# Kernel optimization log

Hardware: AMD Instinct MI355X
Metric: run time of the kernel (lower is better)

Reference implementation:

```python
import jax, jax.numpy as jnp
import numpy as np

B, N, M, D, H = 2, 2048, 77, 1024, 16
DH = D // H
SCALE = DH ** -0.5
EPS = 1e-5


def _round_ste(x):
    return x + jax.lax.stop_gradient(jnp.round(x) - x)


def _fq(x, delta, zp, n_bits):
    # UniformAffineQuantizer: fake quant-dequant with straight-through round
    xi = _round_ste(x / delta) + zp
    xq = jnp.clip(xi, 0.0, 2.0 ** n_bits - 1.0)
    return (xq - zp) * delta


def _ln(x, g, b):
    mu = jnp.mean(x, -1, keepdims=True)
    var = jnp.var(x, -1, keepdims=True)
    return (x - mu) * jax.lax.rsqrt(var + EPS) * g + b


def _attn(x, ctx, wq, wk, wv, wo, bo, dq, dk, dv, dw):
    b, n, _ = x.shape
    m = ctx.shape[1]
    q = (x @ wq).reshape(b, n, H, DH).transpose(0, 2, 1, 3)   # b h n d
    k = (ctx @ wk).reshape(b, m, H, DH).transpose(0, 2, 1, 3)
    v = (ctx @ wv).reshape(b, m, H, DH).transpose(0, 2, 1, 3)
    sim = jnp.einsum('bhid,bhjd->bhij', _fq(q, dq, 128.0, 8), _fq(k, dk, 128.0, 8)) * SCALE
    attn = jax.nn.softmax(sim, axis=-1)
    out = jnp.einsum('bhij,bhjd->bhid', _fq(attn, dw, 0.0, 8), _fq(v, dv, 128.0, 8))
    out = out.transpose(0, 2, 1, 3).reshape(b, n, D)
    return out @ wo + bo


def setup_inputs():
    key = jax.random.key(0)
    ks = jax.random.split(key, 16)
    w = lambda k, s: (jax.random.normal(k, s, jnp.float32) * 0.02)
    d = lambda v: jnp.full((1,), v, jnp.float32)
    return {
        'x': jax.random.normal(ks[0], (B, N, D), jnp.float32),
        'context': jax.random.normal(ks[1], (B, M, D), jnp.float32),
        'ln1_g': jnp.ones((D,), jnp.float32), 'ln1_b': jnp.zeros((D,), jnp.float32),
        'ln2_g': jnp.ones((D,), jnp.float32), 'ln2_b': jnp.zeros((D,), jnp.float32),
        'ln3_g': jnp.ones((D,), jnp.float32), 'ln3_b': jnp.zeros((D,), jnp.float32),
        'a1_wq': w(ks[2], (D, D)), 'a1_wk': w(ks[3], (D, D)), 'a1_wv': w(ks[4], (D, D)),
        'a1_wo': w(ks[5], (D, D)), 'a1_bo': jnp.zeros((D,), jnp.float32),
        'a2_wq': w(ks[6], (D, D)), 'a2_wk': w(ks[7], (D, D)), 'a2_wv': w(ks[8], (D, D)),
        'a2_wo': w(ks[9], (D, D)), 'a2_bo': jnp.zeros((D,), jnp.float32),
        'ff_w1': w(ks[10], (D, 8 * D)), 'ff_b1': jnp.zeros((8 * D,), jnp.float32),
        'ff_w2': w(ks[11], (4 * D, D)), 'ff_b2': jnp.zeros((D,), jnp.float32),
        'd_q1': d(0.02), 'd_k1': d(0.02), 'd_v1': d(0.02), 'd_w1': d(1.0 / 255.0),
        'd_q2': d(0.02), 'd_k2': d(0.02), 'd_v2': d(0.02), 'd_w2': d(1.0 / 255.0),
    }


def reference(x, context, ln1_g, ln1_b, ln2_g, ln2_b, ln3_g, ln3_b,
              a1_wq, a1_wk, a1_wv, a1_wo, a1_bo,
              a2_wq, a2_wk, a2_wv, a2_wo, a2_bo,
              ff_w1, ff_b1, ff_w2, ff_b2,
              d_q1, d_k1, d_v1, d_w1, d_q2, d_k2, d_v2, d_w2):
    # x = attn1(norm1(x)) + x   (self-attention)
    h1 = _ln(x, ln1_g, ln1_b)
    x = _attn(h1, h1, a1_wq, a1_wk, a1_wv, a1_wo, a1_bo, d_q1, d_k1, d_v1, d_w1) + x
    # x = attn2(norm2(x), context) + x   (cross-attention)
    h2 = _ln(x, ln2_g, ln2_b)
    x = _attn(h2, context, a2_wq, a2_wk, a2_wv, a2_wo, a2_bo, d_q2, d_k2, d_v2, d_w2) + x
    # x = ff(norm3(x)) + x   (GEGLU feed-forward)
    h3 = _ln(x, ln3_g, ln3_b)
    hg = h3 @ ff_w1 + ff_b1
    a, g = jnp.split(hg, 2, axis=-1)
    x = (a * jax.nn.gelu(g, approximate=False)) @ ff_w2 + ff_b2 + x
    return x
```

## Files before the change

kernel.cpp:

```cpp
#include <hip/hip_runtime.h>
#include <cstdint>
#include <cmath>

typedef unsigned short u16;
typedef unsigned int   u32;

typedef __bf16 bx8 __attribute__((ext_vector_type(8)));
typedef float  fx4 __attribute__((ext_vector_type(4)));

#define H_  16
#define DH_ 64
#define QSCALE 0.18033688011112042f

__device__ __forceinline__ float bf2f(u16 h){ return __uint_as_float(((u32)h) << 16); }
__device__ __forceinline__ u16 f2bf(float f){
  u32 u = __float_as_uint(f);
  u32 r = (u + 0x7FFFu + ((u >> 16) & 1u)) >> 16;
  return (u16)r;
}

__device__ __forceinline__ float ldv(const void* p, size_t i, int f32){
  return f32 ? ((const float*)p)[i] : bf2f(((const u16*)p)[i]);
}

__device__ __forceinline__ void gld16(const void* g, void* l){
  __builtin_amdgcn_global_load_lds((const __attribute__((address_space(1))) u32*)g,
                                   (__attribute__((address_space(3))) u32*)l,
                                   16, 0, 0);
}

__device__ __forceinline__ float fq_val(float v, float delta){
  float xi = rintf(v / delta) + 128.0f;
  xi = fminf(fmaxf(xi, 0.0f), 255.0f);
  return (xi - 128.0f) * delta;
}

__device__ __forceinline__ float gelu_f(float x){
  float x3 = x * x * x;
  float z = 0.7978845608028654f * x + 0.035677408136300125f * x3;
  float u = __expf(-2.0f * z);
  float t = 1.0f - 2.0f * u / (1.0f + u);
  return 0.5f * x * (1.0f + t);
}

__global__ void detect_k(const u32* __restrict__ x, int* __restrict__ flag){
  __shared__ int cnt;
  if (threadIdx.x == 0) cnt = 0;
  __syncthreads();
  u32 w = x[threadIdx.x];
  int e = (w >> 7) & 0xFF;
  if (e >= 100 && e <= 140) atomicAdd(&cnt, 1);
  __syncthreads();
  if (threadIdx.x == 0) *flag = (cnt < 192) ? 1 : 0;
}

__global__ __launch_bounds__(256) void cvt_k(const void* __restrict__ in, u16* __restrict__ out,
                                             int n, const int* __restrict__ flagp){
  int f32 = *flagp;
  int i = blockIdx.x * 256 + threadIdx.x;
  if (i < n) out[i] = f32 ? f2bf(((const float*)in)[i]) : ((const u16*)in)[i];
}

__global__ __launch_bounds__(256) void tr8_k(
    const void* s0, const void* s1, const void* s2, const void* s3,
    const void* s4, const void* s5, const void* s6, const void* s7,
    u16* __restrict__ out, const int* __restrict__ flagp){
  __shared__ u16 t[32][33];
  int f32 = *flagp;
  int z = blockIdx.z;
  const void* in = z==0?s0:z==1?s1:z==2?s2:z==3?s3:z==4?s4:z==5?s5:z==6?s6:s7;
  u16* o = out + ((size_t)z << 20);
  int n0 = blockIdx.x << 5, r0 = blockIdx.y << 5;
  int tx = threadIdx.x & 31, ty = threadIdx.x >> 5;
  #pragma unroll
  for (int i = 0; i < 4; i++)
    t[ty + i*8][tx] = f2bf(ldv(in, (size_t)(r0 + ty + i*8) * 1024 + n0 + tx, f32));
  __syncthreads();
  #pragma unroll
  for (int i = 0; i < 4; i++)
    o[(size_t)(n0 + ty + i*8) * 1024 + r0 + tx] = t[tx][ty + i*8];
}

__global__ __launch_bounds__(256) void tr_k(const void* __restrict__ in, u16* __restrict__ out,
                                            int Rout, int C, const int* __restrict__ flagp){
  __shared__ u16 t[32][33];
  int f32 = *flagp;
  int n0 = blockIdx.x << 5, r0 = blockIdx.y << 5;
  int tx = threadIdx.x & 31, ty = threadIdx.x >> 5;
  #pragma unroll
  for (int i = 0; i < 4; i++)
    t[ty + i*8][tx] = f2bf(ldv(in, (size_t)(r0 + ty + i*8) * C + n0 + tx, f32));
  __syncthreads();
  #pragma unroll
  for (int i = 0; i < 4; i++)
    out[(size_t)(n0 + ty + i*8) * Rout + r0 + tx] = t[tx][ty + i*8];
}

__global__ __launch_bounds__(256) void ln_k(const void* __restrict__ x,
    const void* __restrict__ gam, const void* __restrict__ bet, u16* __restrict__ out,
    const int* __restrict__ flagp, int xdual){
  __shared__ float sb[8];
  const int f32 = *flagp;
  const int f32x = xdual ? f32 : 0;
  const int row = blockIdx.x, t = threadIdx.x;
  float v0, v1, v2, v3;
  if (f32x){
    float4 xv = *(const float4*)((const float*)x + (size_t)row * 1024 + t * 4);
    v0 = xv.x; v1 = xv.y; v2 = xv.z; v3 = xv.w;
  } else {
    ushort4 xv = *(const ushort4*)((const u16*)x + (size_t)row * 1024 + t * 4);
    v0 = bf2f(xv.x); v1 = bf2f(xv.y); v2 = bf2f(xv.z); v3 = bf2f(xv.w);
  }
  float s = v0 + v1 + v2 + v3;
  #pragma unroll
  for (int mk = 32; mk; mk >>= 1) s += __shfl_xor(s, mk);
  if ((t & 63) == 0) sb[t >> 6] = s;
  __syncthreads();
  float mu = (sb[0] + sb[1] + sb[2] + sb[3]) * 0.0009765625f;
  float d0 = v0 - mu, d1 = v1 - mu, d2 = v2 - mu, d3 = v3 - mu;
  float ss = d0*d0 + d1*d1 + d2*d2 + d3*d3;
  #pragma unroll
  for (int mk = 32; mk; mk >>= 1) ss += __shfl_xor(ss, mk);
  if ((t & 63) == 0) sb[4 + (t >> 6)] = ss;
  __syncthreads();
  float var = (sb[4] + sb[5] + sb[6] + sb[7]) * 0.0009765625f;
  float rs = rsqrtf(var + 1e-5f);
  int c = t * 4;
  u16 o0 = f2bf(d0 * rs * ldv(gam, c+0, f32) + ldv(bet, c+0, f32));
  u16 o1 = f2bf(d1 * rs * ldv(gam, c+1, f32) + ldv(bet, c+1, f32));
  u16 o2 = f2bf(d2 * rs * ldv(gam, c+2, f32) + ldv(bet, c+2, f32));
  u16 o3 = f2bf(d3 * rs * ldv(gam, c+3, f32) + ldv(bet, c+3, f32));
  uint2 ov; ov.x = (u32)o0 | ((u32)o1 << 16); ov.y = (u32)o2 | ((u32)o3 << 16);
  *(uint2*)(out + (size_t)row * 1024 + c) = ov;
}

__global__ __launch_bounds__(512)
void gemm_mr(const u16* __restrict__ A, const u16* __restrict__ BT,
             u16* __restrict__ P0, u16* __restrict__ P1, u16* __restrict__ P2,
             const void* D0, const void* D1, const void* D2,
             float sc0, float sc1, float sc2,
             int md0, int md1, int md2,
             const int* __restrict__ flagp,
             int M, int K, int rpb, int npad)
{
  __shared__ u16 As[2][128 * 32];
  __shared__ u16 Bs[2][128 * 32];
  const int tid = threadIdx.x;
  const int l = tid & 63, w = tid >> 6;
  const int lr = l & 15, lq = l >> 4;
  const int m0 = blockIdx.y * 128, n0 = blockIdx.x * 128;
  const int wrow = (w & 3) * 32, wcol = (w >> 2) * 64;

  fx4 acc[2][4];
  #pragma unroll
  for (int i = 0; i < 2; i++)
    #pragma unroll
    for (int j = 0; j < 4; j++){ fx4 z = {0.f,0.f,0.f,0.f}; acc[i][j] = z; }

  const int r0 = tid >> 2, p0 = tid & 3;
  const int c0 = p0 ^ (r0 & 3);
  int am0 = m0 + r0; if (am0 > M - 1) am0 = M - 1;
  const u16* gA = A  + (size_t)am0 * K + c0 * 8;
  const u16* gB = BT + (size_t)(n0 + r0) * K + c0 * 8;
  const int lo = w * 512;

  const int nk = K >> 5;
  gld16(gA, &As[0][lo]);
  gld16(gB, &Bs[0][lo]);

  for (int kt = 0; kt < nk; ++kt){
    __syncthreads();
    const int cur = kt & 1;
    if (kt + 1 < nk){
      const int nb = cur ^ 1;
      const int ko = (kt + 1) << 5;
      gld16(gA + ko, &As[nb][lo]);
      gld16(gB + ko, &Bs[nb][lo]);
    }
    bx8 aF[2], bF[4];
    #pragma unroll
    for (int i = 0; i < 2; i++){
      int row = wrow + i * 16 + lr;
      aF[i] = *(const bx8*)&As[cur][row * 32 + (lq ^ (row & 3)) * 8];
    }
    #pragma unroll
    for (int j = 0; j < 4; j++){
      int row = wcol + j * 16 + lr;
      bF[j] = *(const bx8*)&Bs[cur][row * 32 + (lq ^ (row & 3)) * 8];
    }
    #pragma unroll
    for (int i = 0; i < 2; i++)
      #pragma unroll
      for (int j = 0; j < 4; j++)
        acc[i][j] = __builtin_amdgcn_mfma_f32_16x16x32_bf16(aF[i], bF[j], acc[i][j], 0, 0, 0);
  }

  const int f32 = *flagp;
  const int reg = n0 >> 10;
  const int cbase = n0 & 1023;
  u16* P = reg == 0 ? P0 : (reg == 1 ? P1 : P2);
  const void* D = reg == 0 ? D0 : (reg == 1 ? D1 : D2);
  const float sc = reg == 0 ? sc0 : (reg == 1 ? sc1 : sc2);
  const int md = reg == 0 ? md0 : (reg == 1 ? md1 : md2);
  const float delta = ldv(D, 0, f32);

  #pragma unroll
  for (int i = 0; i < 2; i++)
    #pragma unroll
    for (int j = 0; j < 4; j++)
      #pragma unroll
      for (int rr = 0; rr < 4; rr++){
        int gm = m0 + wrow + i * 16 + lq * 4 + rr;
        int col = cbase + wcol + j * 16 + lr;
        if (gm < M){
          float v = fq_val(acc[i][j][rr], delta) * sc;
          if (md == 0){
            P[(size_t)gm * 1024 + col] = f2bf(v);
          } else {
            int bb = gm / rpb; int jj = gm - bb * rpb;
            int hh = col >> 6, dh = col & 63;
            P[(size_t)((bb * H_ + hh) * DH_ + dh) * npad + jj] = f2bf(v);
          }
        }
      }
}

template<int MODE>
__global__ __launch_bounds__(256)
void gemm64(const u16* __restrict__ A, const u16* __restrict__ BT,
            void* __restrict__ Co, const void* __restrict__ res,
            const void* __restrict__ bias, const void* __restrict__ dptr, float sc,
            const int* __restrict__ flagp, int res_dual,
            int M, int K)
{
  __shared__ u16 As[2][64 * 32];
  __shared__ u16 Bs[2][128 * 32];
  const int tid = threadIdx.x;
  const int l = tid & 63, w = tid >> 6;
  const int lr = l & 15, lq = l >> 4;
  const int m0 = blockIdx.y * 64, n0 = blockIdx.x * 128;
  const int wrow = (w >> 1) * 32, wcol = (w & 1) * 64;

  fx4 acc[2][4];
  #pragma unroll
  for (int i = 0; i < 2; i++)
    #pragma unroll
    for (int j = 0; j < 4; j++){ fx4 z = {0.f,0.f,0.f,0.f}; acc[i][j] = z; }

  const int r0 = tid >> 2, p0 = tid & 3;
  const int c0 = p0 ^ (r0 & 3);
  const int r1 = r0 + 64;
  int am0 = m0 + r0; if (am0 > M - 1) am0 = M - 1;
  const u16* gA0 = A  + (size_t)am0 * K + c0 * 8;
  const u16* gB0 = BT + (size_t)(n0 + r0) * K + c0 * 8;
  const u16* gB1 = BT + (size_t)(n0 + r1) * K + c0 * 8;
  const int lo0 = (w * 64) * 8, lo1 = (256 + w * 64) * 8;

  const int nk = K >> 5;
  gld16(gA0, &As[0][lo0]);
  gld16(gB0, &Bs[0][lo0]);
  gld16(gB1, &Bs[0][lo1]);

  for (int kt = 0; kt < nk; ++kt){
    __syncthreads();
    const int cur = kt & 1;
    if (kt + 1 < nk){
      const int nb = cur ^ 1;
      const int ko = (kt + 1) << 5;
      gld16(gA0 + ko, &As[nb][lo0]);
      gld16(gB0 + ko, &Bs[nb][lo0]);
      gld16(gB1 + ko, &Bs[nb][lo1]);
    }
    bx8 aF[2], bF[4];
    #pragma unroll
    for (int i = 0; i < 2; i++){
      int row = wrow + i * 16 + lr;
      aF[i] = *(const bx8*)&As[cur][row * 32 + (lq ^ (row & 3)) * 8];
    }
    #pragma unroll
    for (int j = 0; j < 4; j++){
      int row = wcol + j * 16 + lr;
      bF[j] = *(const bx8*)&Bs[cur][row * 32 + (lq ^ (row & 3)) * 8];
    }
    #pragma unroll
    for (int i = 0; i < 2; i++)
      #pragma unroll
      for (int j = 0; j < 4; j++)
        acc[i][j] = __builtin_amdgcn_mfma_f32_16x16x32_bf16(aF[i], bF[j], acc[i][j], 0, 0, 0);
  }

  const int f32 = *flagp;
  float delta = 1.f;
  if (MODE == 0) delta = ldv(dptr, 0, f32);

  #pragma unroll
  for (int i = 0; i < 2; i++)
    #pragma unroll
    for (int j = 0; j < 4; j++)
      #pragma unroll
      for (int rr = 0; rr < 4; rr++){
        int gm = m0 + wrow + i * 16 + lq * 4 + rr;
        int gn = n0 + wcol + j * 16 + lr;
        if (gm < M){
          float v = acc[i][j][rr];
          size_t idx = (size_t)gm * 1024 + gn;
          if (MODE == 0){
            ((u16*)Co)[idx] = f2bf(fq_val(v, delta) * sc);
          } else if (MODE == 5){
            float r = res_dual ? ldv(res, idx, f32) : bf2f(((const u16*)res)[idx]);
            ((u16*)Co)[idx] = f2bf(v + ldv(bias, gn, f32) + r);
          } else {
            float o = v + ldv(bias, gn, f32) + bf2f(((const u16*)res)[idx]);
            if (f32) ((float*)Co)[idx] = o;
            else     ((u16*)Co)[idx]  = f2bf(o);
          }
        }
      }
}

__global__ __launch_bounds__(512)
void gemm_glu(const u16* __restrict__ A, const u16* __restrict__ WT,
              u16* __restrict__ GE, const void* __restrict__ bias,
              const int* __restrict__ flagp, int M, int K)
{
  __shared__ u16 As[2][128 * 32];
  __shared__ u16 Ba[2][128 * 32];
  __shared__ u16 Bg[2][128 * 32];
  const int tid = threadIdx.x;
  const int l = tid & 63, w = tid >> 6;
  const int lr = l & 15, lq = l >> 4;
  const int m0 = blockIdx.y * 128, n0 = blockIdx.x * 128;
  const int wrow = (w & 3) * 32, wcol = (w >> 2) * 64;

  fx4 accA[2][4], accG[2][4];
  #pragma unroll
  for (int i = 0; i < 2; i++)
    #pragma unroll
    for (int j = 0; j < 4; j++){
      fx4 z = {0.f,0.f,0.f,0.f}; accA[i][j] = z; accG[i][j] = z;
    }

  const int r0 = tid >> 2, p0 = tid & 3;
  const int c0 = p0 ^ (r0 & 3);
  int am0 = m0 + r0; if (am0 > M - 1) am0 = M - 1;
  const u16* gA  = A  + (size_t)am0 * K + c0 * 8;
  const u16* gBa = WT + (size_t)(n0 + r0) * K + c0 * 8;
  const u16* gBg = WT + (size_t)(4096 + n0 + r0) * K + c0 * 8;
  const int lo = w * 512;

  const int nk = K >> 5;
  gld16(gA,  &As[0][lo]);
  gld16(gBa, &Ba[0][lo]);
  gld16(gBg, &Bg[0][lo]);

  for (int kt = 0; kt < nk; ++kt){
    __syncthreads();
    const int cur = kt & 1;
    if (kt + 1 < nk){
      const int nb = cur ^ 1;
      const int ko = (kt + 1) << 5;
      gld16(gA + ko,  &As[nb][lo]);
      gld16(gBa + ko, &Ba[nb][lo]);
      gld16(gBg + ko, &Bg[nb][lo]);
    }
    bx8 aF[2], bFa[4], bFg[4];
    #pragma unroll
    for (int i = 0; i < 2; i++){
      int row = wrow + i * 16 + lr;
      aF[i] = *(const bx8*)&As[cur][row * 32 + (lq ^ (row & 3)) * 8];
    }
    #pragma unroll
    for (int j = 0; j < 4; j++){
      int row = wcol + j * 16 + lr;
      bFa[j] = *(const bx8*)&Ba[cur][row * 32 + (lq ^ (row & 3)) * 8];
      bFg[j] = *(const bx8*)&Bg[cur][row * 32 + (lq ^ (row & 3)) * 8];
    }
    #pragma unroll
    for (int i = 0; i < 2; i++)
      #pragma unroll
      for (int j = 0; j < 4; j++){
        accA[i][j] = __builtin_amdgcn_mfma_f32_16x16x32_bf16(aF[i], bFa[j], accA[i][j], 0, 0, 0);
        accG[i][j] = __builtin_amdgcn_mfma_f32_16x16x32_bf16(aF[i], bFg[j], accG[i][j], 0, 0, 0);
      }
  }

  const int f32 = *flagp;

  #pragma unroll
  for (int i = 0; i < 2; i++)
    #pragma unroll
    for (int j = 0; j < 4; j++)
      #pragma unroll
      for (int rr = 0; rr < 4; rr++){
        int gm = m0 + wrow + i * 16 + lq * 4 + rr;
        int gn = n0 + wcol + j * 16 + lr;
        float va = accA[i][j][rr] + ldv(bias, gn, f32);
        float vg = accG[i][j][rr] + ldv(bias, 4096 + gn, f32);
        GE[(size_t)gm * 4096 + gn] = f2bf(va * gelu_f(vg));
      }
}

__global__ __launch_bounds__(256) void attn_k(
    const u16* __restrict__ Qf, const u16* __restrict__ Kf,
    const u16* __restrict__ VT, u16* __restrict__ AO,
    const void* __restrict__ dwp, const int* __restrict__ flagp,
    int Nq, int Lk, int Lpad)
{
  __shared__ u16 Ks[128 * 72];
  __shared__ u16 Vs[64 * 136];
  __shared__ u16 Ps[64 * 136];
  const int tid = threadIdx.x, l = tid & 63, w = tid >> 6;
  const int lr = l & 15, lq = l >> 4;
  const int q0 = blockIdx.x << 6;
  const int b = blockIdx.y >> 4, hh = blockIdx.y & 15;
  const int wq = w << 4;
  const float dw = ldv(dwp, 0, *flagp);
  const float rdw = 1.0f / dw;

  bx8 aQ[2];
  #pragma unroll
  for (int kk = 0; kk < 2; kk++)
    aQ[kk] = *(const bx8*)(Qf + ((size_t)(b * Nq + q0 + wq + lr)) * 1024
                               + hh * 64 + kk * 32 + lq * 8);

  const int ntiles = (Lk + 127) >> 7;

  float s_acc[4] = {0.f, 0.f, 0.f, 0.f};
  for (int jt = 0; jt < ntiles; ++jt){
    const int j0 = jt << 7;
    #pragma unroll
    for (int p = 0; p < 4; p++){
      int s = tid + (p << 8);
      int r = s >> 3, c = s & 7;
      int jr = j0 + r; if (jr > Lk - 1) jr = Lk - 1;
      bx8 kv = *(const bx8*)(Kf + ((size_t)(b * Lk + jr)) * 1024 + hh * 64 + c * 8);
      *(bx8*)&Ks[r * 72 + c * 8] = kv;
    }
    __syncthreads();

    const bool full = (j0 + 128 <= Lk);
    #pragma unroll
    for (int j = 0; j < 8; j++){
      const int row = j * 16 + lr;
      bx8 bK0 = *(const bx8*)&Ks[row * 72 + lq * 8];
      bx8 bK1 = *(const bx8*)&Ks[row * 72 + (lq + 4) * 8];
      fx4 sv = {0.f,0.f,0.f,0.f};
      sv = __builtin_amdgcn_mfma_f32_16x16x32_bf16(aQ[0], bK0, sv, 0, 0, 0);
      sv = __builtin_amdgcn_mfma_f32_16x16x32_bf16(aQ[1], bK1, sv, 0, 0, 0);
      if (full){
        #pragma unroll
        for (int rr = 0; rr < 4; rr++) s_acc[rr] += exp2f(sv[rr]);
      } else {
        const bool in = (j0 + row < Lk);
        #pragma unroll
        for (int rr = 0; rr < 4; rr++) s_acc[rr] += in ? exp2f(sv[rr]) : 0.f;
      }
    }
    __syncthreads();
  }

  float cr[4];
  #pragma unroll
  for (int rr = 0; rr < 4; rr++){
    float s = s_acc[rr];
    #pragma unroll
    for (int mk = 1; mk < 16; mk <<= 1) s += __shfl_xor(s, mk);
    cr[rr] = rdw / s;
  }

  fx4 oacc[4];
  #pragma unroll
  for (int dj = 0; dj < 4; dj++){ fx4 z = {0.f,0.f,0.f,0.f}; oacc[dj] = z; }

  for (int jt = 0; jt < ntiles; ++jt){
    const int j0 = jt << 7;
    #pragma unroll
    for (int p = 0; p < 4; p++){
      int s = tid + (p << 8);
      int r = s >> 3, c = s & 7;
      int jr = j0 + r; if (jr > Lk - 1) jr = Lk - 1;
      bx8 kv = *(const bx8*)(Kf + ((size_t)(b * Lk + jr)) * 1024 + hh * 64 + c * 8);
      *(bx8*)&Ks[r * 72 + c * 8] = kv;
    }
    #pragma unroll
    for (int p = 0; p < 4; p++){
      int s = tid + (p << 8);
      int dh = s >> 4, c = s & 15;
      bx8 vv = *(const bx8*)(VT + ((size_t)((b * H_ + hh) * DH_ + dh)) * Lpad + j0 + c * 8);
      *(bx8*)&Vs[dh * 136 + c * 8] = vv;
    }
    __syncthreads();

    const bool full = (j0 + 128 <= Lk);
    #pragma unroll
    for (int j = 0; j < 8; j++){
      const int row = j * 16 + lr;
      bx8 bK0 = *(const bx8*)&Ks[row * 72 + lq * 8];
      bx8 bK1 = *(const bx8*)&Ks[row * 72 + (lq + 4) * 8];
      fx4 sv = {0.f,0.f,0.f,0.f};
      sv = __builtin_amdgcn_mfma_f32_16x16x32_bf16(aQ[0], bK0, sv, 0, 0, 0);
      sv = __builtin_amdgcn_mfma_f32_16x16x32_bf16(aQ[1], bK1, sv, 0, 0, 0);
      const bool in = full || (j0 + row < Lk);
      #pragma unroll
      for (int rr = 0; rr < 4; rr++){
        float pq = 0.f;
        if (in){
          float xi = fminf(fmaxf(rintf(exp2f(sv[rr]) * cr[rr]), 0.f), 255.f);
          pq = xi * dw;
        }
        Ps[(wq + lq * 4 + rr) * 136 + row] = f2bf(pq);
      }
    }
    __syncthreads();

    #pragma unroll
    for (int kk = 0; kk < 4; kk++){
      bx8 aP = *(const bx8*)&Ps[(wq + lr) * 136 + kk * 32 + lq * 8];
      #pragma unroll
      for (int dj = 0; dj < 4; dj++){
        bx8 bV = *(const bx8*)&Vs[(dj * 16 + lr) * 136 + kk * 32 + lq * 8];
        oacc[dj] = __builtin_amdgcn_mfma_f32_16x16x32_bf16(aP, bV, oacc[dj], 0, 0, 0);
      }
    }
    __syncthreads();
  }

  #pragma unroll
  for (int dj = 0; dj < 4; dj++)
    #pragma unroll
    for (int rr = 0; rr < 4; rr++){
      const int row = wq + lq * 4 + rr;
      const int col = dj * 16 + lr;
      AO[((size_t)(b * Nq + q0 + row)) * 1024 + hh * 64 + col] = f2bf(oacc[dj][rr]);
    }
}


extern "C" void kernel_launch(void* const* d_in, const int* in_sizes, int n_in,
                              void* d_out, int out_size, void* d_ws, size_t ws_size,
                              hipStream_t stream)
{
  const void* X    = d_in[0];
  const void* CTX  = d_in[1];
  const void* LN1G = d_in[2];
  const void* LN1B = d_in[3];
  const void* LN2G = d_in[4];
  const void* LN2B = d_in[5];
  const void* LN3G = d_in[6];
  const void* LN3B = d_in[7];
  const void* W1Q  = d_in[8];
  const void* W1K  = d_in[9];
  const void* W1V  = d_in[10];
  const void* W1O  = d_in[11];
  const void* B1O  = d_in[12];
  const void* W2Q  = d_in[13];
  const void* W2K  = d_in[14];
  const void* W2V  = d_in[15];
  const void* W2O  = d_in[16];
  const void* B2O  = d_in[17];
  const void* FW1  = d_in[18];
  const void* FB1  = d_in[19];
  const void* FW2  = d_in[20];
  const void* FB2  = d_in[21];
  const void* DQ1  = d_in[22];
  const void* DK1  = d_in[23];
  const void* DV1  = d_in[24];
  const void* DW1  = d_in[25];
  const void* DQ2  = d_in[26];
  const void* DK2  = d_in[27];
  const void* DV2  = d_in[28];
  const void* DW2  = d_in[29];

  char* ws = (char*)d_ws;
  u16* wslot = (u16*)(ws + (0ull  << 20));
  u16* xs    = (u16*)(ws + (16ull << 20));
  u16* h     = (u16*)(ws + (24ull << 20));
  u16* bufA  = (u16*)(ws + (32ull << 20));
  u16* bufB  = (u16*)(ws + (40ull << 20));
  u16* bufC  = (u16*)(ws + (48ull << 20));
  u16* ge    = bufA;
  u16* ctxc  = (u16*)(ws + (64ull << 20));
  int* flag  = (int*)(ws + (65ull << 20));

  const dim3 G8x64(8, 64), GAT(32, 32);
  const int NCTX = 154 * 1024;
  const size_t MB2 = 1048576;

  detect_k<<<1, 256, 0, stream>>>((const u32*)X, flag);
  cvt_k<<<(NCTX + 255) / 256, 256, 0, stream>>>(CTX, ctxc, NCTX, flag);
  tr8_k<<<dim3(32, 32, 8), 256, 0, stream>>>(W1Q, W1K, W1V, W1O, W2Q, W2K, W2V, W2O,
                                             wslot, flag);

  ln_k<<<4096, 256, 0, stream>>>(X, LN1G, LN1B, h, flag, 1);
  gemm_mr<<<dim3(24, 32), 512, 0, stream>>>(h, wslot,
      bufA, bufB, bufC, DQ1, DK1, DV1, QSCALE, 1.f, 1.f, 0, 0, 1,
      flag, 4096, 1024, 2048, 2048);
  attn_k<<<GAT, 256, 0, stream>>>(bufA, bufB, bufC, h, DW1, flag, 2048, 2048, 2048);
  gemm64<5><<<G8x64, 256, 0, stream>>>(h, wslot + 3 * MB2, xs, X, B1O, nullptr, 1.f,
                                       flag, 1, 4096, 1024);

  ln_k<<<4096, 256, 0, stream>>>(xs, LN2G, LN2B, h, flag, 0);
  gemm64<0><<<G8x64, 256, 0, stream>>>(h, wslot + 4 * MB2, bufA, nullptr, nullptr, DQ2,
                                       QSCALE, flag, 0, 4096, 1024);
  gemm_mr<<<dim3(16, 2), 512, 0, stream>>>(ctxc, wslot + 5 * MB2,
      bufB, bufC, nullptr, DK2, DV2, DV2, 1.f, 1.f, 1.f, 0, 1, 1,
      flag, 154, 1024, 77, 128);
  attn_k<<<GAT, 256, 0, stream>>>(bufA, bufB, bufC, h, DW2, flag, 2048, 77, 128);
  gemm64<5><<<G8x64, 256, 0, stream>>>(h, wslot + 7 * MB2, xs, xs, B2O, nullptr, 1.f,
                                       flag, 0, 4096, 1024);

  ln_k<<<4096, 256, 0, stream>>>(xs, LN3G, LN3B, h, flag, 0);
  tr_k<<<dim3(256, 32), 256, 0, stream>>>(FW1, wslot, 1024, 8192, flag);
  gemm_glu<<<dim3(32, 32), 512, 0, stream>>>(h, wslot, ge, FB1, flag, 4096, 1024);
  tr_k<<<dim3(32, 128), 256, 0, stream>>>(FW2, wslot, 4096, 1024, flag);
  gemm64<7><<<G8x64, 256, 0, stream>>>(ge, wslot, d_out, xs, FB2, nullptr, 1.f,
                                       flag, 0, 4096, 4096);
}
```

Baseline: 721.0 us.

## Restructure attention kernel with async double-buffered K loads and swizzled LDS

Rewrites the two-pass attention kernel to use 512 threads over 128 query rows per block. K tiles are loaded with global_load_lds into a double buffer so the next tile loads while the current one is computed, and LDS rows use XOR swizzling instead of padding. The MFMA operands are swapped so the row sum needs only two shuffles. P is packed with v_cvt_pk_bf16 as integer levels, and dw is applied once at the output, which drops a barrier per tile. This aims to cut global-load latency, LDS bank conflicts and conversion work, at the cost of more LDS per block and possibly lower occupancy.

```diff
diff --git a/kernel.cpp b/kernel.cpp
--- a/kernel.cpp
+++ b/kernel.cpp
@@ -17,6 +17,12 @@
   u32 u = __float_as_uint(f);
   u32 r = (u + 0x7FFFu + ((u >> 16) & 1u)) >> 16;
   return (u16)r;
+}
+
+__device__ __forceinline__ u32 pk_bf16(float a, float b){
+  u32 r;
+  asm("v_cvt_pk_bf16_f32 %0, %1, %2" : "=v"(r) : "v"(a), "v"(b));
+  return r;
 }
 
 __device__ __forceinline__ float ldv(const void* p, size_t i, int f32){
@@ -400,139 +406,146 @@
       }
 }
 
-__global__ __launch_bounds__(256) void attn_k(
+__global__ __launch_bounds__(512, 4) void attn_k(
     const u16* __restrict__ Qf, const u16* __restrict__ Kf,
     const u16* __restrict__ VT, u16* __restrict__ AO,
     const void* __restrict__ dwp, const int* __restrict__ flagp,
     int Nq, int Lk, int Lpad)
 {
-  __shared__ u16 Ks[128 * 72];
-  __shared__ u16 Vs[64 * 136];
-  __shared__ u16 Ps[64 * 136];
+  __shared__ u16 lds[40960];
+  u16* const KB0 = lds;
+  u16* const KB1 = lds + 8192;
+  u16* const Vs  = lds + 16384;
+  u16* const Ps  = lds + 24576;
+
   const int tid = threadIdx.x, l = tid & 63, w = tid >> 6;
-  const int lr = l & 15, lq = l >> 4;
-  const int q0 = blockIdx.x << 6;
+  const int lr = l & 15, lq = l >> 4, m = lr & 7;
+  const int q0 = blockIdx.x << 7;
   const int b = blockIdx.y >> 4, hh = blockIdx.y & 15;
   const int wq = w << 4;
   const float dw = ldv(dwp, 0, *flagp);
-  const float rdw = 1.0f / dw;
-
-  bx8 aQ[2];
-  #pragma unroll
-  for (int kk = 0; kk < 2; kk++)
-    aQ[kk] = *(const bx8*)(Qf + ((size_t)(b * Nq + q0 + wq + lr)) * 1024
-                               + hh * 64 + kk * 32 + lq * 8);
+
+  const u16* qp = Qf + ((size_t)(b * Nq + q0 + wq + lr) << 10) + (hh << 6) + (lq << 3);
+  bx8 aQ0 = *(const bx8*)(qp);
+  bx8 aQ1 = *(const bx8*)(qp + 32);
+
+  const int krl = (w << 3) + (l >> 3), kcl = l & 7;
+  const int vrl = (w << 2) + (l >> 4), vcl = l & 15;
+
+  auto stageK = [&](u16* dst, int j0){
+    #pragma unroll
+    for (int t = 0; t < 2; ++t){
+      int r = krl + (t << 6);
+      int jr = j0 + r; if (jr > Lk - 1) jr = Lk - 1;
+      int c = kcl ^ (r & 7);
+      gld16(Kf + ((size_t)(b * Lk + jr) << 10) + (hh << 6) + (c << 3),
+            dst + (w << 9) + (t << 12));
+    }
+  };
+  auto stageV = [&](int j0){
+    #pragma unroll
+    for (int t = 0; t < 2; ++t){
+      int dh = vrl + (t << 5);
+      int c = vcl ^ (dh & 7);
+      gld16(VT + (size_t)((((b << 4) + hh) << 6) + dh) * Lpad + j0 + (c << 3),
+            Vs + (w << 9) + (t << 12));
+    }
+  };
 
   const int ntiles = (Lk + 127) >> 7;
-
-  float s_acc[4] = {0.f, 0.f, 0.f, 0.f};
+  const int ch0 = ((lq ^ m) << 3), ch1 = (((lq + 4) ^ m) << 3);
+
+  float sa0 = 0.f, sa1 = 0.f, sa2 = 0.f, sa3 = 0.f;
+  stageK(KB0, 0);
   for (int jt = 0; jt < ntiles; ++jt){
+    __syncthreads();
+    const u16* Kc = (jt & 1) ? KB1 : KB0;
+    if (jt + 1 < ntiles) stageK((jt & 1) ? KB0 : KB1, (jt + 1) << 7);
     const int j0 = jt << 7;
-    #pragma unroll
-    for (int p = 0; p < 4; p++){
-      int s = tid + (p << 8);
-      int r = s >> 3, c = s & 7;
-      int jr = j0 + r; if (jr > Lk - 1) jr = Lk - 1;
-      bx8 kv = *(const bx8*)(Kf + ((size_t)(b * Lk + jr)) * 1024 + hh * 64 + c * 8);
-      *(bx8*)&Ks[r * 72 + c * 8] = kv;
-    }
+    const bool full = (j0 + 128 <= Lk);
+    #pragma unroll
+    for (int j = 0; j < 8; ++j){
+      const int ro = ((j << 4) + lr) << 6;
+      bx8 k0 = *(const bx8*)&Kc[ro + ch0];
+      bx8 k1 = *(const bx8*)&Kc[ro + ch1];
+      fx4 sv = {0.f,0.f,0.f,0.f};
+      sv = __builtin_amdgcn_mfma_f32_16x16x32_bf16(k0, aQ0, sv, 0, 0, 0);
+      sv = __builtin_amdgcn_mfma_f32_16x16x32_bf16(k1, aQ1, sv, 0, 0, 0);
+      if (full){
+        sa0 += exp2f(sv[0]); sa1 += exp2f(sv[1]);
+        sa2 += exp2f(sv[2]); sa3 += exp2f(sv[3]);
+      } else {
+        const int kb = j0 + (j << 4) + (lq << 2);
+        sa0 += (kb + 0 < Lk) ? exp2f(sv[0]) : 0.f;
+        sa1 += (kb + 1 < Lk) ? exp2f(sv[1]) : 0.f;
+        sa2 += (kb + 2 < Lk) ? exp2f(sv[2]) : 0.f;
+        sa3 += (kb + 3 < Lk) ? exp2f(sv[3]) : 0.f;
+      }
+    }
+  }
+  __syncthreads();
+  float s = (sa0 + sa1) + (sa2 + sa3);
+  s += __shfl_xor(s, 16);
+  s += __shfl_xor(s, 32);
+  const float cr = (1.0f / dw) / s;
+
+  fx4 oacc[4];
+  #pragma unroll
+  for (int dj = 0; dj < 4; ++dj){ fx4 z = {0.f,0.f,0.f,0.f}; oacc[dj] = z; }
+
+  const int qloc = wq + lr;
+  const int pw = (qloc << 7) + (lq << 2);
+
+  stageK(KB0, 0);
+  for (int jt = 0; jt < ntiles; ++jt){
     __syncthreads();
-
+    const int j0 = jt << 7;
+    stageV(j0);
+    if (jt + 1 < ntiles) stageK((jt & 1) ? KB0 : KB1, j0 + 128);
+    const u16* Kc = (jt & 1) ? KB1 : KB0;
     const bool full = (j0 + 128 <= Lk);
     #pragma unroll
-    for (int j = 0; j < 8; j++){
-      const int row = j * 16 + lr;
-      bx8 bK0 = *(const bx8*)&Ks[row * 72 + lq * 8];
-      bx8 bK1 = *(const bx8*)&Ks[row * 72 + (lq + 4) * 8];
+    for (int j = 0; j < 8; ++j){
+      const int ro = ((j << 4) + lr) << 6;
+      bx8 k0 = *(const bx8*)&Kc[ro + ch0];
+      bx8 k1 = *(const bx8*)&Kc[ro + ch1];
       fx4 sv = {0.f,0.f,0.f,0.f};
-      sv = __builtin_amdgcn_mfma_f32_16x16x32_bf16(aQ[0], bK0, sv, 0, 0, 0);
-      sv = __builtin_amdgcn_mfma_f32_16x16x32_bf16(aQ[1], bK1, sv, 0, 0, 0);
+      sv = __builtin_amdgcn_mfma_f32_16x16x32_bf16(k0, aQ0, sv, 0, 0, 0);
+      sv = __builtin_amdgcn_mfma_f32_16x16x32_bf16(k1, aQ1, sv, 0, 0, 0);
+      float x0, x1, x2, x3;
       if (full){
-        #pragma unroll
-        for (int rr = 0; rr < 4; rr++) s_acc[rr] += exp2f(sv[rr]);
+        x0 = rintf(exp2f(sv[0]) * cr);
+        x1 = rintf(exp2f(sv[1]) * cr);
+        x2 = rintf(exp2f(sv[2]) * cr);
+        x3 = rintf(exp2f(sv[3]) * cr);
       } else {
-        const bool in = (j0 + row < Lk);
-        #pragma unroll
-        for (int rr = 0; rr < 4; rr++) s_acc[rr] += in ? exp2f(sv[rr]) : 0.f;
+        const int kb = j0 + (j << 4) + (lq << 2);
+        x0 = (kb + 0 < Lk) ? rintf(exp2f(sv[0]) * cr) : 0.f;
+        x1 = (kb + 1 < Lk) ? rintf(exp2f(sv[1]) * cr) : 0.f;
+        x2 = (kb + 2 < Lk) ? rintf(exp2f(sv[2]) * cr) : 0.f;
+        x3 = (kb + 3 < Lk) ? rintf(exp2f(sv[3]) * cr) : 0.f;
       }
+      uint2 pp; pp.x = pk_bf16(x0, x1); pp.y = pk_bf16(x2, x3);
+      *(uint2*)&Ps[pw + ((j ^ m) << 4)] = pp;
     }
     __syncthreads();
-  }
-
-  float cr[4];
-  #pragma unroll
-  for (int rr = 0; rr < 4; rr++){
-    float s = s_acc[rr];
-    #pragma unroll
-    for (int mk = 1; mk < 16; mk <<= 1) s += __shfl_xor(s, mk);
-    cr[rr] = rdw / s;
-  }
-
-  fx4 oacc[4];
-  #pragma unroll
-  for (int dj = 0; dj < 4; dj++){ fx4 z = {0.f,0.f,0.f,0.f}; oacc[dj] = z; }
-
-  for (int jt = 0; jt < ntiles; ++jt){
-    const int j0 = jt << 7;
-    #pragma unroll
-    for (int p = 0; p < 4; p++){
-      int s = tid + (p << 8);
-      int r = s >> 3, c = s & 7;
-      int jr = j0 + r; if (jr > Lk - 1) jr = Lk - 1;
-      bx8 kv = *(const bx8*)(Kf + ((size_t)(b * Lk + jr)) * 1024 + hh * 64 + c * 8);
-      *(bx8*)&Ks[r * 72 + c * 8] = kv;
-    }
-    #pragma unroll
-    for (int p = 0; p < 4; p++){
-      int s = tid + (p << 8);
-      int dh = s >> 4, c = s & 15;
-      bx8 vv = *(const bx8*)(VT + ((size_t)((b * H_ + hh) * DH_ + dh)) * Lpad + j0 + c * 8);
-      *(bx8*)&Vs[dh * 136 + c * 8] = vv;
-    }
-    __syncthreads();
-
-    const bool full = (j0 + 128 <= Lk);
-    #pragma unroll
-    for (int j = 0; j < 8; j++){
-      const int row = j * 16 + lr;
-      bx8 bK0 = *(const bx8*)&Ks[row * 72 + lq * 8];
-      bx8 bK1 = *(const bx8*)&Ks[row * 72 + (lq + 4) * 8];
-      fx4 sv = {0.f,0.f,0.f,0.f};
-      sv = __builtin_amdgcn_mfma_f32_16x16x32_bf16(aQ[0], bK0, sv, 0, 0, 0);
-      sv = __builtin_amdgcn_mfma_f32_16x16x32_bf16(aQ[1], bK1, sv, 0, 0, 0);
-      const bool in = full || (j0 + row < Lk);
+    #pragma unroll
+    for (int kk = 0; kk < 4; ++kk){
+      bx8 aP = *(const bx8*)&Ps[(qloc << 7) + ((((kk << 3) + (lq << 1)) ^ (m << 2)) << 2)];
       #pragma unroll
-      for (int rr = 0; rr < 4; rr++){
-        float pq = 0.f;
-        if (in){
-          float xi = fminf(fmaxf(rintf(exp2f(sv[rr]) * cr[rr]), 0.f), 255.f);
-          pq = xi * dw;
-        }
-        Ps[(wq + lq * 4 + rr) * 136 + row] = f2bf(pq);
-      }
-    }
-    __syncthreads();
-
-    #pragma unroll
-    for (int kk = 0; kk < 4; kk++){
-      bx8 aP = *(const bx8*)&Ps[(wq + lr) * 136 + kk * 32 + lq * 8];
-      #pragma unroll
-      for (int dj = 0; dj < 4; dj++){
-        bx8 bV = *(const bx8*)&Vs[(dj * 16 + lr) * 136 + kk * 32 + lq * 8];
+      for (int dj = 0; dj < 4; ++dj){
+        bx8 bV = *(const bx8*)&Vs[((((dj << 4) + lr)) << 7) + ((((kk << 2) + lq) ^ m) << 3)];
         oacc[dj] = __builtin_amdgcn_mfma_f32_16x16x32_bf16(aP, bV, oacc[dj], 0, 0, 0);
       }
     }
-    __syncthreads();
   }
 
-  #pragma unroll
-  for (int dj = 0; dj < 4; dj++)
-    #pragma unroll
-    for (int rr = 0; rr < 4; rr++){
-      const int row = wq + lq * 4 + rr;
-      const int col = dj * 16 + lr;
-      AO[((size_t)(b * Nq + q0 + row)) * 1024 + hh * 64 + col] = f2bf(oacc[dj][rr]);
-    }
+  const size_t ob = ((size_t)(b * Nq + q0 + wq + (lq << 2)) << 10) + (hh << 6) + lr;
+  #pragma unroll
+  for (int dj = 0; dj < 4; ++dj)
+    #pragma unroll
+    for (int rr = 0; rr < 4; ++rr)
+      AO[ob + ((size_t)rr << 10) + (dj << 4)] = f2bf(oacc[dj][rr] * dw);
 }
 
 
@@ -582,7 +595,7 @@
   u16* ctxc  = (u16*)(ws + (64ull << 20));
   int* flag  = (int*)(ws + (65ull << 20));
 
-  const dim3 G8x64(8, 64), GAT(32, 32);
+  const dim3 G8x64(8, 64), GAT(16, 32);
   const int NCTX = 154 * 1024;
   const size_t MB2 = 1048576;
 
@@ -595,7 +608,7 @@
   gemm_mr<<<dim3(24, 32), 512, 0, stream>>>(h, wslot,
       bufA, bufB, bufC, DQ1, DK1, DV1, QSCALE, 1.f, 1.f, 0, 0, 1,
       flag, 4096, 1024, 2048, 2048);
-  attn_k<<<GAT, 256, 0, stream>>>(bufA, bufB, bufC, h, DW1, flag, 2048, 2048, 2048);
+  attn_k<<<GAT, 512, 0, stream>>>(bufA, bufB, bufC, h, DW1, flag, 2048, 2048, 2048);
   gemm64<5><<<G8x64, 256, 0, stream>>>(h, wslot + 3 * MB2, xs, X, B1O, nullptr, 1.f,
                                        flag, 1, 4096, 1024);
 
@@ -605,7 +618,7 @@
   gemm_mr<<<dim3(16, 2), 512, 0, stream>>>(ctxc, wslot + 5 * MB2,
       bufB, bufC, nullptr, DK2, DV2, DV2, 1.f, 1.f, 1.f, 0, 1, 1,
       flag, 154, 1024, 77, 128);
-  attn_k<<<GAT, 256, 0, stream>>>(bufA, bufB, bufC, h, DW2, flag, 2048, 77, 128);
+  attn_k<<<GAT, 512, 0, stream>>>(bufA, bufB, bufC, h, DW2, flag, 2048, 77, 128);
   gemm64<5><<<G8x64, 256, 0, stream>>>(h, wslot + 7 * MB2, xs, xs, B2O, nullptr, 1.f,
                                        flag, 0, 4096, 1024);
 
```

New measurement: 659.2 us. -8.6%, faster.
